# Optimization experiments

Measured on AMD Instinct MI355X. Metric: run time of the kernel, lower is better.

The kernel has to match this reference:

```python
import jax, jax.numpy as jnp
import numpy as np

TOKENS = 16384
IN_F = 2048
OUT_F = 2048
RANK = 32
GROUP = 64          # int4 scale group size
PAD = 256           # token padding multiple used by the fused activation quantizer
QMAX = 7.0          # signed int4 symmetric quantization


def setup_inputs() -> dict:
    key = jax.random.key(0)
    ks = jax.random.split(key, 7)
    x = jax.random.normal(ks[0], (TOKENS, IN_F), dtype=jnp.float32)
    # packed int4 weights: two signed nibbles per int8 lane
    qweight = jax.random.randint(ks[1], (OUT_F, IN_F // 2), -128, 128, dtype=jnp.int8)
    # per-group weight scales [in//group, out], strictly positive
    wscales = jnp.abs(jax.random.normal(ks[2], (IN_F // GROUP, OUT_F), dtype=jnp.float32)) * 0.01 + 1e-4
    # activation smoothing factors, positive and near 1
    smooth_factor = jnp.abs(jax.random.normal(ks[3], (IN_F,), dtype=jnp.float32)) * 0.5 + 0.75
    bias = jax.random.normal(ks[4], (OUT_F,), dtype=jnp.float32) * 0.01
    proj_down = jax.random.normal(ks[5], (IN_F, RANK), dtype=jnp.float32) * 0.02
    proj_up = jax.random.normal(ks[6], (OUT_F, RANK), dtype=jnp.float32) * 0.02
    return {"x": x, "qweight": qweight, "wscales": wscales,
            "smooth_factor": smooth_factor, "bias": bias,
            "proj_down": proj_down, "proj_up": proj_up}


def _unpack_int4(qweight):
    # low nibble = even input channel, high nibble = odd input channel; arithmetic shifts keep sign
    low = jnp.right_shift(jnp.left_shift(qweight, 4), 4)
    high = jnpp = jnp.right_shift(qweight, 4)
    w = jnp.stack([low, high], axis=-1).reshape(qweight.shape[0], qweight.shape[1] * 2)
    return w.astype(jnp.float32)  # [out, in], values in [-8, 7]


def _forward(x, qweight, wscales, smooth_factor, bias, proj_down, proj_up):
    T = x.shape[0]
    t_pad = ((T + PAD - 1) // PAD) * PAD
    # activation smoothing
    xs = x / smooth_factor
    xs_p = jnp.pad(xs, ((0, t_pad - T), (0, 0)))
    # per-token per-64-group symmetric int4 activation quantization
    xg = xs_p.reshape(t_pad, IN_F // GROUP, GROUP)
    amax = jnp.max(jnp.abs(xg), axis=-1)                       # [Tp, G]
    ascales = jnp.where(amax > 0, amax / QMAX, jnp.float32(1.0))
    qx = jnp.clip(jnp.round(xg / ascales[..., None]), -8.0, 7.0)
    xdq = (qx * ascales[..., None]).reshape(t_pad, IN_F)       # dequantized activations
    # dequantize packed int4 weights with per-group scales
    w = _unpack_int4(qweight)                                  # [out, in]
    wdq = (w.reshape(OUT_F, IN_F // GROUP, GROUP) * wscales.T[:, :, None]).reshape(OUT_F, IN_F)
    # packed GEMM (dequantized equivalent) + fused low-rank residual + bias
    y = xdq @ wdq.T                                            # [Tp, out]
    y = y + (xs_p @ proj_down) @ proj_up.T + bias
    return y[:T]


def reference(x, qweight, wscales, smooth_factor, bias, proj_down, proj_up):
    return _forward(x, qweight, wscales, smooth_factor, bias, proj_down, proj_up)
```

## Files before the change

### kernel.cpp

```cpp
#include <hip/hip_runtime.h>

#define TOKENS 16384
#define THALF 8192
#define INF 2048
#define OUTF 2048
#define RANK 32
#define BM 256
#define BN 128
#define NPER 32

typedef int   int32x4  __attribute__((ext_vector_type(4)));
typedef int   int32x2  __attribute__((ext_vector_type(2)));
typedef float floatx4  __attribute__((ext_vector_type(4)));
typedef short bf16x8   __attribute__((ext_vector_type(8)));
typedef _Float16 f16x8 __attribute__((ext_vector_type(8)));

typedef __attribute__((address_space(1))) const void gconst_t;
typedef __attribute__((address_space(3))) void ldsv_t;

__device__ __forceinline__ void gload_lds16(const void* g, void* l) {
  __builtin_amdgcn_global_load_lds((gconst_t*)g, (ldsv_t*)l, 16, 0, 0);
}

__device__ __forceinline__ unsigned short f2bf(float f) {
  unsigned u = __float_as_uint(f);
  unsigned r = (u + 0x7FFFu + ((u >> 16) & 1u)) >> 16;
  return (unsigned short)r;
}

__global__ __launch_bounds__(256) void unpack_kernel(const int* __restrict__ qw,
                                                     const float* __restrict__ wsc,
                                                     _Float16* __restrict__ wdq) {
  int idx = blockIdx.x * 256 + threadIdx.x;
  int o = idx >> 6;
  int ch = idx & 63;
  float ws = wsc[(size_t)(ch >> 1) * OUTF + o];
  const int4* src = (const int4*)qw + (size_t)idx * 4;
  _Float16* dst = wdq + (size_t)o * INF + ch * 32;
#pragma unroll
  for (int q = 0; q < 4; ++q) {
    int4 v = src[q];
    int e[4] = {v.x, v.y, v.z, v.w};
    alignas(16) _Float16 h[8];
#pragma unroll
    for (int j = 0; j < 4; ++j) {
      int lo = ((int)((unsigned)e[j] << 28)) >> 28;
      int hi = ((int)((unsigned)e[j] << 24)) >> 28;
      h[2 * j]     = (_Float16)((float)lo * ws);
      h[2 * j + 1] = (_Float16)((float)hi * ws);
    }
    *(int4*)(dst + q * 8) = *(const int4*)h;
  }
}

__global__ __launch_bounds__(256) void prep_pdT(const float* __restrict__ pd,
                                                unsigned short* __restrict__ pdT) {
  int idx = blockIdx.x * 256 + threadIdx.x;
  int r = idx >> 11, c = idx & 2047;
  pdT[idx] = f2bf(pd[(size_t)c * RANK + r]);
}

__global__ __launch_bounds__(256) void quant_kernel(
    const float* __restrict__ x, const float* __restrict__ smooth,
    const unsigned short* __restrict__ pdT,
    _Float16* __restrict__ xdq, float* __restrict__ tdown, int tbase) {
  __shared__ char lds[32768];
  int tid = threadIdx.x, lane = tid & 63, wid = tid >> 6;
  int t0rel = blockIdx.x * 32;
  int mi = wid >> 1, ni = wid & 1;
  floatx4 acc = {0.f, 0.f, 0.f, 0.f};

  floatx4 xv[8];
  floatx4 sm;
  int32x4 pv[4];

  auto issue_loads = [&](int kc) {
    const float* xb = x + (size_t)(tbase + t0rel + wid * 8) * INF + kc * 256 + lane * 4;
#pragma unroll
    for (int r = 0; r < 8; ++r) xv[r] = *(const floatx4*)(xb + r * INF);
    sm = *(const floatx4*)(smooth + kc * 256 + lane * 4);
#pragma unroll
    for (int q = 0; q < 4; ++q) {
      int flat = tid + q * 256;
      int row = flat >> 5, c16 = flat & 31;
      pv[q] = *(const int32x4*)((const char*)pdT + (size_t)row * 4096 + kc * 512 + c16 * 16);
    }
  };

  issue_loads(0);

  for (int kc = 0; kc < 8; ++kc) {
    floatx4 rsm;
    rsm[0] = 1.0f / sm[0]; rsm[1] = 1.0f / sm[1];
    rsm[2] = 1.0f / sm[2]; rsm[3] = 1.0f / sm[3];
#pragma unroll
    for (int q = 0; q < 4; ++q) {
      int flat = tid + q * 256;
      int row = flat >> 5, c16 = flat & 31;
      int byte = (row * 512 + c16 * 16) ^ ((row & 7) << 4);
      *(int32x4*)(lds + 16384 + byte) = pv[q];
    }
#pragma unroll
    for (int r = 0; r < 8; ++r) {
      floatx4 xs;
      xs[0] = xv[r][0] * rsm[0]; xs[1] = xv[r][1] * rsm[1];
      xs[2] = xv[r][2] * rsm[2]; xs[3] = xv[r][3] * rsm[3];
      float m4 = fmaxf(fmaxf(fabsf(xs[0]), fabsf(xs[1])),
                       fmaxf(fabsf(xs[2]), fabsf(xs[3])));
      m4 = fmaxf(m4, __shfl_xor(m4, 1, 64));
      m4 = fmaxf(m4, __shfl_xor(m4, 2, 64));
      m4 = fmaxf(m4, __shfl_xor(m4, 4, 64));
      m4 = fmaxf(m4, __shfl_xor(m4, 8, 64));
      float ascale = m4 > 0.f ? m4 / 7.0f : 1.0f;
      float rq = 1.0f / ascale;
      int tokrel = t0rel + wid * 8 + r;
      alignas(8) _Float16 hq[4];
#pragma unroll
      for (int b = 0; b < 4; ++b) {
        float qf = fminf(7.f, fmaxf(-8.f, rintf(xs[b] * rq)));
        hq[b] = (_Float16)(qf * ascale);
      }
      *(int32x2*)((char*)xdq + ((size_t)tokrel * INF + kc * 256 + lane * 4) * 2) =
          *(const int32x2*)hq;
      unsigned lo = (unsigned)f2bf(xs[0]) | ((unsigned)f2bf(xs[1]) << 16);
      unsigned hi = (unsigned)f2bf(xs[2]) | ((unsigned)f2bf(xs[3]) << 16);
      int lrow = wid * 8 + r;
      int xbyte = (lrow * 512 + lane * 8) ^ ((lrow & 7) << 4);
      int32x2 wv; wv[0] = (int)lo; wv[1] = (int)hi;
      *(int32x2*)(lds + xbyte) = wv;
    }
    __syncthreads();
    if (kc + 1 < 8) issue_loads(kc + 1);
#pragma unroll
    for (int ks = 0; ks < 8; ++ks) {
      int arow = mi * 16 + (lane & 15);
      int ab = (arow * 512 + ks * 64 + ((lane >> 4) << 4)) ^ ((arow & 7) << 4);
      bf16x8 av = *(const bf16x8*)(lds + ab);
      int brow = ni * 16 + (lane & 15);
      int bb = (brow * 512 + ks * 64 + ((lane >> 4) << 4)) ^ ((brow & 7) << 4);
      bf16x8 bv = *(const bf16x8*)(lds + 16384 + bb);
      acc = __builtin_amdgcn_mfma_f32_16x16x32_bf16(av, bv, acc, 0, 0, 0);
    }
    __syncthreads();
  }

  int trow = tbase + t0rel + mi * 16 + ((lane >> 4) << 2);
  int col = ni * 16 + (lane & 15);
#pragma unroll
  for (int r = 0; r < 4; ++r)
    tdown[(size_t)(trow + r) * RANK + col] = acc[r];
}

__global__ __launch_bounds__(512, 2) void gemm_kernel(
    const _Float16* __restrict__ xdq, const _Float16* __restrict__ wdq,
    const float* __restrict__ tdown, const float* __restrict__ pu,
    const float* __restrict__ bias, float* __restrict__ y,
    int tbase, int mPanels) {
  __shared__ char smem[147456];

  int tid = threadIdx.x;
  int lane = tid & 63;
  int wid = tid >> 6;
  int wm = wid >> 1, wn = wid & 1;

  int s = blockIdx.x;
  int xcd = s & 7, idx = s >> 3;
  int npan = ((xcd & 3) << 2) + (idx & 3);
  int mpan = (xcd >> 2) * (mPanels >> 1) + (idx >> 2);
  int o0 = npan * BN;
  int t0rel = mpan * BM;
  int t0abs = tbase + t0rel;

  floatx4 acc[4][4];
#pragma unroll
  for (int m = 0; m < 4; ++m)
#pragma unroll
    for (int n = 0; n < 4; ++n) acc[m][n] = (floatx4){0.f, 0.f, 0.f, 0.f};

  auto stage = [&](int g) {
    int bufb = (g % 3) * 49152;
#pragma unroll
    for (int i = 0; i < 4; ++i) {
      int f = i * 512 + tid;
      int row = f >> 3, sl = (f & 7) ^ (row & 7);
      gload_lds16((const char*)xdq + (size_t)(t0rel + row) * (INF * 2) + g * 128 + sl * 16,
                  smem + bufb + i * 8192 + wid * 1024);
    }
#pragma unroll
    for (int i = 0; i < 2; ++i) {
      int f = i * 512 + tid;
      int row = f >> 3, sl = (f & 7) ^ (row & 7);
      gload_lds16((const char*)wdq + (size_t)(o0 + row) * (INF * 2) + g * 128 + sl * 16,
                  smem + bufb + 32768 + i * 8192 + wid * 1024);
    }
  };

  int aoff[4][2], boff[4][2];
#pragma unroll
  for (int mr = 0; mr < 4; ++mr) {
    int r = (wm << 6) + (mr << 4) + (lane & 15);
#pragma unroll
    for (int ks = 0; ks < 2; ++ks) {
      int sl = ((ks << 2) + (lane >> 4)) ^ (r & 7);
      aoff[mr][ks] = r * 128 + sl * 16;
    }
  }
#pragma unroll
  for (int nr = 0; nr < 4; ++nr) {
    int r = (wn << 6) + (nr << 4) + (lane & 15);
#pragma unroll
    for (int ks = 0; ks < 2; ++ks) {
      int sl = ((ks << 2) + (lane >> 4)) ^ (r & 7);
      boff[nr][ks] = 32768 + r * 128 + sl * 16;
    }
  }

  stage(0);
  stage(1);

  for (int g = 0; g < NPER; ++g) {
    if (g == NPER - 1) asm volatile("s_waitcnt vmcnt(0)" ::: "memory");
    else               asm volatile("s_waitcnt vmcnt(6)" ::: "memory");
    __builtin_amdgcn_s_barrier();
    __builtin_amdgcn_sched_barrier(0);

    if (g + 2 < NPER) stage(g + 2);

    int bufb = (g % 3) * 49152;
    f16x8 af[2][4], bf_[2][4];
#pragma unroll
    for (int ks = 0; ks < 2; ++ks) {
#pragma unroll
      for (int mr = 0; mr < 4; ++mr) af[ks][mr] = *(const f16x8*)(smem + bufb + aoff[mr][ks]);
#pragma unroll
      for (int nr = 0; nr < 4; ++nr) bf_[ks][nr] = *(const f16x8*)(smem + bufb + boff[nr][ks]);
    }

#pragma unroll
    for (int ks = 0; ks < 2; ++ks)
#pragma unroll
      for (int mr = 0; mr < 4; ++mr)
#pragma unroll
        for (int nr = 0; nr < 4; ++nr)
          acc[mr][nr] = __builtin_amdgcn_mfma_f32_16x16x32_f16(af[ks][mr], bf_[ks][nr],
                                                               acc[mr][nr], 0, 0, 0);
  }

  __syncthreads();

  unsigned short* td_lds = (unsigned short*)smem;
  unsigned short* pu_lds = (unsigned short*)(smem + 16384);
  {
    int row = tid >> 1, h = (tid & 1) * 16;
    const float* ts = tdown + (size_t)(t0abs + row) * RANK + h;
    unsigned tw[8];
#pragma unroll
    for (int q = 0; q < 4; ++q) {
      float4 v = *(const float4*)(ts + q * 4);
      tw[q * 2 + 0] = (unsigned)f2bf(v.x) | ((unsigned)f2bf(v.y) << 16);
      tw[q * 2 + 1] = (unsigned)f2bf(v.z) | ((unsigned)f2bf(v.w) << 16);
    }
    int4 s0, s1;
    s0.x = (int)tw[0]; s0.y = (int)tw[1]; s0.z = (int)tw[2]; s0.w = (int)tw[3];
    s1.x = (int)tw[4]; s1.y = (int)tw[5]; s1.z = (int)tw[6]; s1.w = (int)tw[7];
    *(int4*)(td_lds + row * 32 + h) = s0;
    *(int4*)(td_lds + row * 32 + h + 8) = s1;
    if (tid < 256) {
      const float* ps = pu + (size_t)(o0 + row) * RANK + h;
      unsigned pw[8];
#pragma unroll
      for (int q = 0; q < 4; ++q) {
        float4 p = *(const float4*)(ps + q * 4);
        pw[q * 2 + 0] = (unsigned)f2bf(p.x) | ((unsigned)f2bf(p.y) << 16);
        pw[q * 2 + 1] = (unsigned)f2bf(p.z) | ((unsigned)f2bf(p.w) << 16);
      }
      s0.x = (int)pw[0]; s0.y = (int)pw[1]; s0.z = (int)pw[2]; s0.w = (int)pw[3];
      s1.x = (int)pw[4]; s1.y = (int)pw[5]; s1.z = (int)pw[6]; s1.w = (int)pw[7];
      *(int4*)(pu_lds + row * 32 + h) = s0;
      *(int4*)(pu_lds + row * 32 + h + 8) = s1;
    }
  }
  __syncthreads();

  bf16x8 ta[4], pb4[4];
  int koff8 = (lane >> 4) << 3;
#pragma unroll
  for (int m = 0; m < 4; ++m)
    ta[m] = *(const bf16x8*)&td_lds[((wm << 6) + (m << 4) + (lane & 15)) * 32 + koff8];
#pragma unroll
  for (int n = 0; n < 4; ++n)
    pb4[n] = *(const bf16x8*)&pu_lds[((wn << 6) + (n << 4) + (lane & 15)) * 32 + koff8];

#pragma unroll
  for (int n = 0; n < 4; ++n) {
    int oc = o0 + (wn << 6) + (n << 4) + (lane & 15);
    float bv = bias[oc];
#pragma unroll
    for (int m = 0; m < 4; ++m) {
      floatx4 c = acc[m][n];
      c = __builtin_amdgcn_mfma_f32_16x16x32_bf16(ta[m], pb4[n], c, 0, 0, 0);
#pragma unroll
      for (int r = 0; r < 4; ++r) {
        int tr = t0abs + (wm << 6) + (m << 4) + ((lane >> 4) << 2) + r;
        y[(size_t)tr * OUTF + oc] = c[r] + bv;
      }
    }
  }
}

extern "C" void kernel_launch(void* const* d_in, const int* in_sizes, int n_in,
                              void* d_out, int out_size, void* d_ws, size_t ws_size,
                              hipStream_t stream) {
  const float* x      = (const float*)d_in[0];
  const int*   qw     = (const int*)d_in[1];
  const float* wsc    = (const float*)d_in[2];
  const float* smooth = (const float*)d_in[3];
  const float* bias   = (const float*)d_in[4];
  const float* pd     = (const float*)d_in[5];
  const float* pu     = (const float*)d_in[6];
  float* y = (float*)d_out;

  char* ws = (char*)d_ws;
  unsigned short* pdT = (unsigned short*)((char*)d_out + (64u << 20));

  if (ws_size >= 77594624ULL) {
    _Float16* xdq = (_Float16*)ws;
    _Float16* wdq = (_Float16*)(ws + 67108864);
    float* tdown  = (float*)(ws + 67108864 + 8388608);
    unpack_kernel<<<512, 256, 0, stream>>>(qw, wsc, wdq);
    prep_pdT<<<256, 256, 0, stream>>>(pd, pdT);
    quant_kernel<<<TOKENS / 32, 256, 0, stream>>>(x, smooth, pdT, xdq, tdown, 0);
    gemm_kernel<<<16 * (TOKENS / BM), 512, 0, stream>>>(
        xdq, wdq, tdown, pu, bias, y, 0, TOKENS / BM);
  } else {
    _Float16* xdq = (_Float16*)ws;
    _Float16* wdq = (_Float16*)(ws + 33554432);
    float* tdown  = (float*)(ws + 33554432 + 8388608);
    unpack_kernel<<<512, 256, 0, stream>>>(qw, wsc, wdq);
    prep_pdT<<<256, 256, 0, stream>>>(pd, pdT);
    for (int c = 0; c < 2; ++c) {
      int tbase = c * THALF;
      quant_kernel<<<THALF / 32, 256, 0, stream>>>(x, smooth, pdT, xdq, tdown, tbase);
      gemm_kernel<<<16 * (THALF / BM), 512, 0, stream>>>(
          xdq, wdq, tdown, pu, bias, y, tbase, THALF / BM);
    }
  }
}
```

Before: 220.8 us.

## Split K-step into two halves interleaving prefetch, LDS reads and MFMA with setprio

Each 64-wide K iteration is split into two 32-wide sub-steps. Each sub-step issues half of the next-next tile's global-to-LDS loads, reads its own fragments, and runs 16 MFMAs at raised wave priority, with an extra barrier between the halves. The aim is to spread memory issue across the loop and keep the matrix pipes fed, in the style of ping-pong scheduling. The cost is an additional barrier and explicit lgkmcnt waits per iteration, and the vmcnt(6) accounting still relies on six loads per stage.

```diff
diff --git a/kernel.cpp b/kernel.cpp
--- a/kernel.cpp
+++ b/kernel.cpp
@@ -177,21 +177,21 @@
 #pragma unroll
     for (int n = 0; n < 4; ++n) acc[m][n] = (floatx4){0.f, 0.f, 0.f, 0.f};
 
-  auto stage = [&](int g) {
+  auto stage_half = [&](int g, int h) {
     int bufb = (g % 3) * 49152;
 #pragma unroll
-    for (int i = 0; i < 4; ++i) {
-      int f = i * 512 + tid;
+    for (int i = 0; i < 2; ++i) {
+      int ii = h * 2 + i;
+      int f = ii * 512 + tid;
       int row = f >> 3, sl = (f & 7) ^ (row & 7);
       gload_lds16((const char*)xdq + (size_t)(t0rel + row) * (INF * 2) + g * 128 + sl * 16,
-                  smem + bufb + i * 8192 + wid * 1024);
-    }
-#pragma unroll
-    for (int i = 0; i < 2; ++i) {
-      int f = i * 512 + tid;
+                  smem + bufb + ii * 8192 + wid * 1024);
+    }
+    {
+      int f = h * 512 + tid;
       int row = f >> 3, sl = (f & 7) ^ (row & 7);
       gload_lds16((const char*)wdq + (size_t)(o0 + row) * (INF * 2) + g * 128 + sl * 16,
-                  smem + bufb + 32768 + i * 8192 + wid * 1024);
+                  smem + bufb + 32768 + h * 8192 + wid * 1024);
     }
   };
 
@@ -215,8 +215,8 @@
     }
   }
 
-  stage(0);
-  stage(1);
+  stage_half(0, 0); stage_half(0, 1);
+  stage_half(1, 0); stage_half(1, 1);
 
   for (int g = 0; g < NPER; ++g) {
     if (g == NPER - 1) asm volatile("s_waitcnt vmcnt(0)" ::: "memory");
@@ -224,26 +224,41 @@
     __builtin_amdgcn_s_barrier();
     __builtin_amdgcn_sched_barrier(0);
 
-    if (g + 2 < NPER) stage(g + 2);
-
     int bufb = (g % 3) * 49152;
-    f16x8 af[2][4], bf_[2][4];
-#pragma unroll
-    for (int ks = 0; ks < 2; ++ks) {
-#pragma unroll
-      for (int mr = 0; mr < 4; ++mr) af[ks][mr] = *(const f16x8*)(smem + bufb + aoff[mr][ks]);
-#pragma unroll
-      for (int nr = 0; nr < 4; ++nr) bf_[ks][nr] = *(const f16x8*)(smem + bufb + boff[nr][ks]);
-    }
-
-#pragma unroll
-    for (int ks = 0; ks < 2; ++ks)
-#pragma unroll
-      for (int mr = 0; mr < 4; ++mr)
-#pragma unroll
-        for (int nr = 0; nr < 4; ++nr)
-          acc[mr][nr] = __builtin_amdgcn_mfma_f32_16x16x32_f16(af[ks][mr], bf_[ks][nr],
-                                                               acc[mr][nr], 0, 0, 0);
+    bool pf = (g + 2 < NPER);
+
+    if (pf) stage_half(g + 2, 0);
+    f16x8 a0[4], b0[4];
+#pragma unroll
+    for (int mr = 0; mr < 4; ++mr) a0[mr] = *(const f16x8*)(smem + bufb + aoff[mr][0]);
+#pragma unroll
+    for (int nr = 0; nr < 4; ++nr) b0[nr] = *(const f16x8*)(smem + bufb + boff[nr][0]);
+    asm volatile("s_waitcnt lgkmcnt(0)" ::: "memory");
+    __builtin_amdgcn_sched_barrier(0);
+    __builtin_amdgcn_s_setprio(1);
+#pragma unroll
+    for (int mr = 0; mr < 4; ++mr)
+#pragma unroll
+      for (int nr = 0; nr < 4; ++nr)
+        acc[mr][nr] = __builtin_amdgcn_mfma_f32_16x16x32_f16(a0[mr], b0[nr], acc[mr][nr], 0, 0, 0);
+    __builtin_amdgcn_s_setprio(0);
+    __builtin_amdgcn_s_barrier();
+
+    if (pf) stage_half(g + 2, 1);
+    f16x8 a1[4], b1[4];
+#pragma unroll
+    for (int mr = 0; mr < 4; ++mr) a1[mr] = *(const f16x8*)(smem + bufb + aoff[mr][1]);
+#pragma unroll
+    for (int nr = 0; nr < 4; ++nr) b1[nr] = *(const f16x8*)(smem + bufb + boff[nr][1]);
+    asm volatile("s_waitcnt lgkmcnt(0)" ::: "memory");
+    __builtin_amdgcn_sched_barrier(0);
+    __builtin_amdgcn_s_setprio(1);
+#pragma unroll
+    for (int mr = 0; mr < 4; ++mr)
+#pragma unroll
+      for (int nr = 0; nr < 4; ++nr)
+        acc[mr][nr] = __builtin_amdgcn_mfma_f32_16x16x32_f16(a1[mr], b1[nr], acc[mr][nr], 0, 0, 0);
+    __builtin_amdgcn_s_setprio(0);
   }
 
   __syncthreads();
```

New measurement: 219.4 us. No clear change (-0.7%).

## Enlarge GEMM tile to 256x256 with four-phase interleaved double-buffered pipeline

Applied to the files above, without the earlier changes.

The GEMM block tile grows from 256x128 to 256x256 with a 2x4 wave layout, so each wave holds a 128x64 accumulator. The triple-buffered LDS pipeline becomes a double buffer in which the A and B halves are staged in four sub-phases, each overlapped with a quarter of the MFMA work under s_setprio. The larger tile raises arithmetic intensity and halves the grid, but it doubles accumulator registers per thread and leaves only two LDS buffers to hide load latency.

```diff
diff --git a/kernel.cpp b/kernel.cpp
--- a/kernel.cpp
+++ b/kernel.cpp
@@ -6,7 +6,7 @@
 #define OUTF 2048
 #define RANK 32
 #define BM 256
-#define BN 128
+#define BN 256
 #define NPER 32
 
 typedef int   int32x4  __attribute__((ext_vector_type(4)));
@@ -156,94 +156,147 @@
     const float* __restrict__ tdown, const float* __restrict__ pu,
     const float* __restrict__ bias, float* __restrict__ y,
     int tbase, int mPanels) {
-  __shared__ char smem[147456];
+  __shared__ char smem[131072];
 
   int tid = threadIdx.x;
   int lane = tid & 63;
   int wid = tid >> 6;
-  int wm = wid >> 1, wn = wid & 1;
+  int wm = wid >> 2, wn = wid & 3;
 
   int s = blockIdx.x;
   int xcd = s & 7, idx = s >> 3;
-  int npan = ((xcd & 3) << 2) + (idx & 3);
-  int mpan = (xcd >> 2) * (mPanels >> 1) + (idx >> 2);
+  int npan = ((xcd & 3) << 1) + (idx & 1);
+  int mpan = (xcd >> 2) * (mPanels >> 1) + (idx >> 1);
   int o0 = npan * BN;
   int t0rel = mpan * BM;
   int t0abs = tbase + t0rel;
 
-  floatx4 acc[4][4];
-#pragma unroll
-  for (int m = 0; m < 4; ++m)
+  floatx4 acc[8][4];
+#pragma unroll
+  for (int m = 0; m < 8; ++m)
 #pragma unroll
     for (int n = 0; n < 4; ++n) acc[m][n] = (floatx4){0.f, 0.f, 0.f, 0.f};
 
-  auto stage = [&](int g) {
-    int bufb = (g % 3) * 49152;
-#pragma unroll
-    for (int i = 0; i < 4; ++i) {
-      int f = i * 512 + tid;
-      int row = f >> 3, sl = (f & 7) ^ (row & 7);
-      gload_lds16((const char*)xdq + (size_t)(t0rel + row) * (INF * 2) + g * 128 + sl * 16,
-                  smem + bufb + i * 8192 + wid * 1024);
-    }
+  auto stageA = [&](int g, int h) {
+    int dst = (g & 1) * 65536 + h * 16384;
 #pragma unroll
     for (int i = 0; i < 2; ++i) {
       int f = i * 512 + tid;
       int row = f >> 3, sl = (f & 7) ^ (row & 7);
-      gload_lds16((const char*)wdq + (size_t)(o0 + row) * (INF * 2) + g * 128 + sl * 16,
-                  smem + bufb + 32768 + i * 8192 + wid * 1024);
+      gload_lds16((const char*)xdq + (size_t)(t0rel + h * 128 + row) * (INF * 2) + g * 128 + sl * 16,
+                  smem + dst + i * 8192 + wid * 1024);
     }
   };
-
-  int aoff[4][2], boff[4][2];
-#pragma unroll
-  for (int mr = 0; mr < 4; ++mr) {
-    int r = (wm << 6) + (mr << 4) + (lane & 15);
-#pragma unroll
-    for (int ks = 0; ks < 2; ++ks) {
-      int sl = ((ks << 2) + (lane >> 4)) ^ (r & 7);
-      aoff[mr][ks] = r * 128 + sl * 16;
-    }
-  }
-#pragma unroll
-  for (int nr = 0; nr < 4; ++nr) {
-    int r = (wn << 6) + (nr << 4) + (lane & 15);
-#pragma unroll
-    for (int ks = 0; ks < 2; ++ks) {
-      int sl = ((ks << 2) + (lane >> 4)) ^ (r & 7);
-      boff[nr][ks] = 32768 + r * 128 + sl * 16;
-    }
-  }
-
-  stage(0);
-  stage(1);
-
-  for (int g = 0; g < NPER; ++g) {
-    if (g == NPER - 1) asm volatile("s_waitcnt vmcnt(0)" ::: "memory");
-    else               asm volatile("s_waitcnt vmcnt(6)" ::: "memory");
+  auto stageB = [&](int g, int h) {
+    int dst = (g & 1) * 65536 + 32768 + h * 16384;
+#pragma unroll
+    for (int i = 0; i < 2; ++i) {
+      int f = i * 512 + tid;
+      int row = f >> 3, sl = (f & 7) ^ (row & 7);
+      gload_lds16((const char*)wdq + (size_t)(o0 + h * 128 + row) * (INF * 2) + g * 128 + sl * 16,
+                  smem + dst + i * 8192 + wid * 1024);
+    }
+  };
+
+  int l = lane & 15;
+  int abase[2], bbase[2];
+#pragma unroll
+  for (int ks = 0; ks < 2; ++ks) {
+    abase[ks] = wm * 16384 + l * 128 + ((((ks << 2) + (lane >> 4)) ^ (l & 7)) << 4);
+    bbase[ks] = 32768 + (wn >> 1) * 16384 + ((wn & 1) * 64 + l) * 128 +
+                ((((ks << 2) + (lane >> 4)) ^ (l & 7)) << 4);
+  }
+
+  stageB(0, 0); stageA(0, 0); stageB(0, 1); stageA(0, 1);
+  stageB(1, 0); stageA(1, 0);
+
+  f16x8 areg[4][2], breg0[2][2], breg1[2][2];
+
+  for (int t = 0; t < NPER; ++t) {
+    if (t == NPER - 1) asm volatile("s_waitcnt vmcnt(0)" ::: "memory");
+    else               asm volatile("s_waitcnt vmcnt(4)" ::: "memory");
     __builtin_amdgcn_s_barrier();
     __builtin_amdgcn_sched_barrier(0);
 
-    if (g + 2 < NPER) stage(g + 2);
-
-    int bufb = (g % 3) * 49152;
-    f16x8 af[2][4], bf_[2][4];
-#pragma unroll
-    for (int ks = 0; ks < 2; ++ks) {
-#pragma unroll
-      for (int mr = 0; mr < 4; ++mr) af[ks][mr] = *(const f16x8*)(smem + bufb + aoff[mr][ks]);
-#pragma unroll
-      for (int nr = 0; nr < 4; ++nr) bf_[ks][nr] = *(const f16x8*)(smem + bufb + boff[nr][ks]);
-    }
-
-#pragma unroll
-    for (int ks = 0; ks < 2; ++ks)
-#pragma unroll
-      for (int mr = 0; mr < 4; ++mr)
-#pragma unroll
-        for (int nr = 0; nr < 4; ++nr)
-          acc[mr][nr] = __builtin_amdgcn_mfma_f32_16x16x32_f16(af[ks][mr], bf_[ks][nr],
-                                                               acc[mr][nr], 0, 0, 0);
+    const char* sb = smem + (t & 1) * 65536;
+    const char* pa0 = sb + abase[0];
+    const char* pa1 = sb + abase[1];
+    const char* pb0 = sb + bbase[0];
+    const char* pb1 = sb + bbase[1];
+
+#pragma unroll
+    for (int j = 0; j < 4; ++j) {
+      areg[j][0] = *(const f16x8*)(pa0 + j * 2048);
+      areg[j][1] = *(const f16x8*)(pa1 + j * 2048);
+    }
+#pragma unroll
+    for (int nf = 0; nf < 2; ++nf) {
+      breg0[nf][0] = *(const f16x8*)(pb0 + nf * 2048);
+      breg0[nf][1] = *(const f16x8*)(pb1 + nf * 2048);
+    }
+    if (t + 1 < NPER) stageB(t + 1, 1);
+    asm volatile("s_waitcnt lgkmcnt(0)" ::: "memory");
+    __builtin_amdgcn_sched_barrier(0);
+    __builtin_amdgcn_s_setprio(1);
+#pragma unroll
+    for (int j = 0; j < 4; ++j)
+#pragma unroll
+      for (int nf = 0; nf < 2; ++nf) {
+        acc[j][nf] = __builtin_amdgcn_mfma_f32_16x16x32_f16(areg[j][0], breg0[nf][0], acc[j][nf], 0, 0, 0);
+        acc[j][nf] = __builtin_amdgcn_mfma_f32_16x16x32_f16(areg[j][1], breg0[nf][1], acc[j][nf], 0, 0, 0);
+      }
+    __builtin_amdgcn_s_setprio(0);
+    __builtin_amdgcn_s_barrier();
+
+#pragma unroll
+    for (int nf = 0; nf < 2; ++nf) {
+      breg1[nf][0] = *(const f16x8*)(pb0 + (2 + nf) * 2048);
+      breg1[nf][1] = *(const f16x8*)(pb1 + (2 + nf) * 2048);
+    }
+    if (t + 1 < NPER) stageA(t + 1, 1);
+    asm volatile("s_waitcnt lgkmcnt(0)" ::: "memory");
+    __builtin_amdgcn_sched_barrier(0);
+    __builtin_amdgcn_s_setprio(1);
+#pragma unroll
+    for (int j = 0; j < 4; ++j)
+#pragma unroll
+      for (int nf = 0; nf < 2; ++nf) {
+        acc[j][2 + nf] = __builtin_amdgcn_mfma_f32_16x16x32_f16(areg[j][0], breg1[nf][0], acc[j][2 + nf], 0, 0, 0);
+        acc[j][2 + nf] = __builtin_amdgcn_mfma_f32_16x16x32_f16(areg[j][1], breg1[nf][1], acc[j][2 + nf], 0, 0, 0);
+      }
+    __builtin_amdgcn_s_setprio(0);
+    __builtin_amdgcn_s_barrier();
+
+#pragma unroll
+    for (int j = 0; j < 4; ++j) {
+      areg[j][0] = *(const f16x8*)(pa0 + (4 + j) * 2048);
+      areg[j][1] = *(const f16x8*)(pa1 + (4 + j) * 2048);
+    }
+    if (t + 2 < NPER) stageB(t + 2, 0);
+    asm volatile("s_waitcnt lgkmcnt(0)" ::: "memory");
+    __builtin_amdgcn_sched_barrier(0);
+    __builtin_amdgcn_s_setprio(1);
+#pragma unroll
+    for (int j = 0; j < 4; ++j)
+#pragma unroll
+      for (int nf = 0; nf < 2; ++nf) {
+        acc[4 + j][2 + nf] = __builtin_amdgcn_mfma_f32_16x16x32_f16(areg[j][0], breg1[nf][0], acc[4 + j][2 + nf], 0, 0, 0);
+        acc[4 + j][2 + nf] = __builtin_amdgcn_mfma_f32_16x16x32_f16(areg[j][1], breg1[nf][1], acc[4 + j][2 + nf], 0, 0, 0);
+      }
+    __builtin_amdgcn_s_setprio(0);
+    __builtin_amdgcn_s_barrier();
+
+    if (t + 2 < NPER) stageA(t + 2, 0);
+    __builtin_amdgcn_s_setprio(1);
+#pragma unroll
+    for (int j = 0; j < 4; ++j)
+#pragma unroll
+      for (int nf = 0; nf < 2; ++nf) {
+        acc[4 + j][nf] = __builtin_amdgcn_mfma_f32_16x16x32_f16(areg[j][0], breg0[nf][0], acc[4 + j][nf], 0, 0, 0);
+        acc[4 + j][nf] = __builtin_amdgcn_mfma_f32_16x16x32_f16(areg[j][1], breg0[nf][1], acc[4 + j][nf], 0, 0, 0);
+      }
+    __builtin_amdgcn_s_setprio(0);
+    __builtin_amdgcn_s_barrier();
   }
 
   __syncthreads();
@@ -253,40 +306,34 @@
   {
     int row = tid >> 1, h = (tid & 1) * 16;
     const float* ts = tdown + (size_t)(t0abs + row) * RANK + h;
-    unsigned tw[8];
+    const float* ps = pu + (size_t)(o0 + row) * RANK + h;
+    unsigned tw[8], pw[8];
 #pragma unroll
     for (int q = 0; q < 4; ++q) {
       float4 v = *(const float4*)(ts + q * 4);
       tw[q * 2 + 0] = (unsigned)f2bf(v.x) | ((unsigned)f2bf(v.y) << 16);
       tw[q * 2 + 1] = (unsigned)f2bf(v.z) | ((unsigned)f2bf(v.w) << 16);
+      float4 p = *(const float4*)(ps + q * 4);
+      pw[q * 2 + 0] = (unsigned)f2bf(p.x) | ((unsigned)f2bf(p.y) << 16);
+      pw[q * 2 + 1] = (unsigned)f2bf(p.z) | ((unsigned)f2bf(p.w) << 16);
     }
     int4 s0, s1;
     s0.x = (int)tw[0]; s0.y = (int)tw[1]; s0.z = (int)tw[2]; s0.w = (int)tw[3];
     s1.x = (int)tw[4]; s1.y = (int)tw[5]; s1.z = (int)tw[6]; s1.w = (int)tw[7];
     *(int4*)(td_lds + row * 32 + h) = s0;
     *(int4*)(td_lds + row * 32 + h + 8) = s1;
-    if (tid < 256) {
-      const float* ps = pu + (size_t)(o0 + row) * RANK + h;
-      unsigned pw[8];
-#pragma unroll
-      for (int q = 0; q < 4; ++q) {
-        float4 p = *(const float4*)(ps + q * 4);
-        pw[q * 2 + 0] = (unsigned)f2bf(p.x) | ((unsigned)f2bf(p.y) << 16);
-        pw[q * 2 + 1] = (unsigned)f2bf(p.z) | ((unsigned)f2bf(p.w) << 16);
-      }
-      s0.x = (int)pw[0]; s0.y = (int)pw[1]; s0.z = (int)pw[2]; s0.w = (int)pw[3];
-      s1.x = (int)pw[4]; s1.y = (int)pw[5]; s1.z = (int)pw[6]; s1.w = (int)pw[7];
-      *(int4*)(pu_lds + row * 32 + h) = s0;
-      *(int4*)(pu_lds + row * 32 + h + 8) = s1;
-    }
+    s0.x = (int)pw[0]; s0.y = (int)pw[1]; s0.z = (int)pw[2]; s0.w = (int)pw[3];
+    s1.x = (int)pw[4]; s1.y = (int)pw[5]; s1.z = (int)pw[6]; s1.w = (int)pw[7];
+    *(int4*)(pu_lds + row * 32 + h) = s0;
+    *(int4*)(pu_lds + row * 32 + h + 8) = s1;
   }
   __syncthreads();
 
-  bf16x8 ta[4], pb4[4];
+  bf16x8 ta[8], pb4[4];
   int koff8 = (lane >> 4) << 3;
 #pragma unroll
-  for (int m = 0; m < 4; ++m)
-    ta[m] = *(const bf16x8*)&td_lds[((wm << 6) + (m << 4) + (lane & 15)) * 32 + koff8];
+  for (int m = 0; m < 8; ++m)
+    ta[m] = *(const bf16x8*)&td_lds[((wm << 7) + (m << 4) + (lane & 15)) * 32 + koff8];
 #pragma unroll
   for (int n = 0; n < 4; ++n)
     pb4[n] = *(const bf16x8*)&pu_lds[((wn << 6) + (n << 4) + (lane & 15)) * 32 + koff8];
@@ -296,12 +343,12 @@
     int oc = o0 + (wn << 6) + (n << 4) + (lane & 15);
     float bv = bias[oc];
 #pragma unroll
-    for (int m = 0; m < 4; ++m) {
+    for (int m = 0; m < 8; ++m) {
       floatx4 c = acc[m][n];
       c = __builtin_amdgcn_mfma_f32_16x16x32_bf16(ta[m], pb4[n], c, 0, 0, 0);
 #pragma unroll
       for (int r = 0; r < 4; ++r) {
-        int tr = t0abs + (wm << 6) + (m << 4) + ((lane >> 4) << 2) + r;
+        int tr = t0abs + (wm << 7) + (m << 4) + ((lane >> 4) << 2) + r;
         y[(size_t)tr * OUTF + oc] = c[r] + bv;
       }
     }
@@ -330,7 +377,7 @@
     unpack_kernel<<<512, 256, 0, stream>>>(qw, wsc, wdq);
     prep_pdT<<<256, 256, 0, stream>>>(pd, pdT);
     quant_kernel<<<TOKENS / 32, 256, 0, stream>>>(x, smooth, pdT, xdq, tdown, 0);
-    gemm_kernel<<<16 * (TOKENS / BM), 512, 0, stream>>>(
+    gemm_kernel<<<8 * (TOKENS / BM), 512, 0, stream>>>(
         xdq, wdq, tdown, pu, bias, y, 0, TOKENS / BM);
   } else {
     _Float16* xdq = (_Float16*)ws;
@@ -341,7 +388,7 @@
     for (int c = 0; c < 2; ++c) {
       int tbase = c * THALF;
       quant_kernel<<<THALF / 32, 256, 0, stream>>>(x, smooth, pdT, xdq, tdown, tbase);
-      gemm_kernel<<<16 * (THALF / BM), 512, 0, stream>>>(
+      gemm_kernel<<<8 * (THALF / BM), 512, 0, stream>>>(
           xdq, wdq, tdown, pu, bias, y, tbase, THALF / BM);
     }
   }
```

Result: faster. 196.4 us (-11.1%).
